# Optimization experiments

Hardware: AMD Instinct MI355X
Metric: run time of the kernel (lower is better)

Reference implementation:

```python
import jax, jax.numpy as jnp
import numpy as np
import math

EMB_DIM = 1024
HEAD_SIZE = 64
T = 4096
B = 4

def setup_inputs() -> dict:
    key = jax.random.key(0)
    k1, k2, k3, k4 = jax.random.split(key, 4)
    scale = 1.0 / math.sqrt(EMB_DIM)
    return {
        "input": jax.random.normal(k1, (B, T, EMB_DIM), dtype=jnp.float32),
        "Wq": jax.random.normal(k2, (EMB_DIM, HEAD_SIZE), dtype=jnp.float32) * scale,
        "Wk": jax.random.normal(k3, (EMB_DIM, HEAD_SIZE), dtype=jnp.float32) * scale,
        "Wv": jax.random.normal(k4, (EMB_DIM, HEAD_SIZE), dtype=jnp.float32) * scale,
    }

def reference(input, Wq, Wk, Wv):
    # q,k,v: [B,T,H]
    q = input @ Wq
    k = input @ Wk
    v = input @ Wv
    # scores: [B,T,T]
    match = jnp.einsum('bqh,bkh->bqk', q, k)
    # 'encoder' mask in this repo = causal tril mask
    causal = jnp.tril(jnp.ones((T, T), dtype=bool))
    match = jnp.where(causal, match, -jnp.inf)
    # NOTE: faithful to source quirk: softmax first, THEN divide by sqrt(head_size)
    attention = jax.nn.softmax(match, axis=-1) / math.sqrt(HEAD_SIZE)
    return jnp.einsum('bqk,bkh->bqh', attention, v)
```

## Files before the change

### kernel.cpp

```cpp
#include <hip/hip_runtime.h>

#define T_SEQ 4096
#define NBATCH 4
#define EMB 1024
#define HS 64
#define BT (NBATCH * T_SEQ)

typedef float f32x4 __attribute__((ext_vector_type(4)));
typedef short s16x8 __attribute__((ext_vector_type(8)));

__device__ __forceinline__ unsigned short f2bf(float x) {
  union { float f; unsigned u; } c; c.f = x;
  unsigned r = c.u + 0x7FFF + ((c.u >> 16) & 1);
  return (unsigned short)(r >> 16);
}
__device__ __forceinline__ float bf2f(unsigned short h) {
  union { unsigned u; float f; } c; c.u = ((unsigned)h) << 16;
  return c.f;
}
__device__ __forceinline__ void cvt8(float4 a0, float4 a1, s16x8& hi, s16x8& lo) {
  float xv[8] = {a0.x, a0.y, a0.z, a0.w, a1.x, a1.y, a1.z, a1.w};
#pragma unroll
  for (int j = 0; j < 8; ++j) {
    unsigned short h = f2bf(xv[j]);
    hi[j] = (short)h;
    lo[j] = (short)f2bf(xv[j] - bf2f(h));
  }
}

__global__ __launch_bounds__(256) void wconv(
    const float* __restrict__ Wq, const float* __restrict__ Wk,
    const float* __restrict__ Wv, unsigned short* __restrict__ wt_hi,
    unsigned short* __restrict__ wt_lo) {
  const int n3 = blockIdx.x;
  const int which = n3 >> 6, n = n3 & 63;
  const float* W = (which == 0) ? Wq : (which == 1) ? Wk : Wv;
#pragma unroll
  for (int i = 0; i < 4; ++i) {
    int k = i * 256 + threadIdx.x;
    float x = W[(size_t)k * HS + n];
    unsigned short h = f2bf(x);
    wt_hi[(size_t)n3 * EMB + k] = h;
    wt_lo[(size_t)n3 * EMB + k] = f2bf(x - bf2f(h));
  }
}

__global__ __launch_bounds__(512) void qkv_mfma(
    const float* __restrict__ inp, const unsigned short* __restrict__ wt_hi,
    const unsigned short* __restrict__ wt_lo, float* __restrict__ qf,
    unsigned short* __restrict__ khi, unsigned short* __restrict__ klo,
    unsigned short* __restrict__ vtb) {
  __shared__ unsigned short Bhi[192 * 40];
  __shared__ unsigned short Blo[192 * 40];
  const int t = threadIdx.x, lane = t & 63, w = t >> 6;
  const int m = lane & 15, quad = lane >> 4;
  const int mg = w >> 2, ng = w & 3;
  const int tok0 = blockIdx.x * 32;
  const int arow = tok0 + mg * 16 + m;

  f32x4 acc[3];
#pragma unroll
  for (int nt = 0; nt < 3; ++nt) acc[nt] = (f32x4){0.f, 0.f, 0.f, 0.f};

  const size_t offa = (size_t)(t >> 2) * EMB + (t & 3) * 8;
  const int idxb = (t < 256) ? (t + 512) : (t - 256);
  const unsigned short* srcb = (t < 256) ? wt_hi : wt_lo;
  const size_t offb = (size_t)(idxb >> 2) * EMB + (idxb & 3) * 8;
  const int idxc = t + 256;
  const size_t offc = (size_t)(idxc >> 2) * EMB + (idxc & 3) * 8;

  uint4 bpa, bpb, bpc;
  float4 apre0, apre1;
  bpa = *(const uint4*)&wt_hi[offa];
  bpb = *(const uint4*)&srcb[offb];
  bpc = *(const uint4*)&wt_lo[offc];
  {
    const float* ap = &inp[(size_t)arow * EMB + quad * 8];
    apre0 = *(const float4*)ap;
    apre1 = *(const float4*)(ap + 4);
  }

  for (int kc = 0; kc < 32; ++kc) {
    const int k0n = (kc + 1) * 32;
    __syncthreads();
    {
      *(uint4*)&Bhi[(t >> 2) * 40 + (t & 3) * 8] = bpa;
      unsigned short* dstb = (t < 256) ? Bhi : Blo;
      *(uint4*)&dstb[(idxb >> 2) * 40 + (idxb & 3) * 8] = bpb;
      *(uint4*)&Blo[(idxc >> 2) * 40 + (idxc & 3) * 8] = bpc;
    }
    __syncthreads();

    s16x8 ah, al;
    cvt8(apre0, apre1, ah, al);

    if (kc < 31) {
      bpa = *(const uint4*)&wt_hi[offa + k0n];
      bpb = *(const uint4*)&srcb[offb + k0n];
      bpc = *(const uint4*)&wt_lo[offc + k0n];
      const float* ap = &inp[(size_t)arow * EMB + k0n + quad * 8];
      apre0 = *(const float4*)ap;
      apre1 = *(const float4*)(ap + 4);
    }

#pragma unroll
    for (int nt = 0; nt < 3; ++nt) {
      int n3 = ng * 48 + nt * 16 + m;
      s16x8 bh = *(const s16x8*)&Bhi[n3 * 40 + quad * 8];
      s16x8 bl = *(const s16x8*)&Blo[n3 * 40 + quad * 8];
      acc[nt] = __builtin_amdgcn_mfma_f32_16x16x32_bf16(ah, bh, acc[nt], 0, 0, 0);
      acc[nt] = __builtin_amdgcn_mfma_f32_16x16x32_bf16(ah, bl, acc[nt], 0, 0, 0);
      acc[nt] = __builtin_amdgcn_mfma_f32_16x16x32_bf16(al, bh, acc[nt], 0, 0, 0);
    }
  }

#pragma unroll
  for (int nt = 0; nt < 3; ++nt) {
    int n3 = ng * 48 + nt * 16 + m;
    int which = n3 >> 6, col = n3 & 63;
#pragma unroll
    for (int r = 0; r < 4; ++r) {
      int tok = tok0 + mg * 16 + quad * 4 + r;
      float val = acc[nt][r];
      if (which == 0) {
        qf[(size_t)tok * HS + col] = val;
      } else if (which == 1) {
        unsigned short h = f2bf(val);
        khi[(size_t)tok * HS + col] = h;
        klo[(size_t)tok * HS + col] = f2bf(val - bf2f(h));
      } else {
        vtb[(size_t)(tok >> 6) * 4096 + (size_t)col * 64 + (tok & 63)] = f2bf(val);
      }
    }
  }
}

__global__ __launch_bounds__(256) void attn_part(
    const float* __restrict__ q, const unsigned short* __restrict__ khi,
    const unsigned short* __restrict__ klo, const unsigned short* __restrict__ vt,
    unsigned short* __restrict__ partO, float* __restrict__ partML) {
  __shared__ unsigned short Khi_s[64 * 72];
  __shared__ unsigned short Klo_s[64 * 72];
  __shared__ unsigned short Vt_s[64 * 72];
  __shared__ unsigned short P_s[4 * 16 * 72];
  const int t = threadIdx.x;
  const int lane = t & 63, w = t >> 6;
  const int m = lane & 15, quad = lane >> 4;

  int u = blockIdx.x;
  const int b = u / 160;
  u -= b * 160;
  int qtile = 0, c = 0;
  {
    int acc2 = 0;
    for (int qq = 0; qq < 64; ++qq) {
      int ncq = (qq >> 4) + 1;
      if (u < acc2 + ncq) { qtile = qq; c = u - acc2; break; }
      acc2 += ncq;
    }
  }
  const int kt0 = c * 16;
  const int kt1 = (kt0 + 16 < qtile + 1) ? kt0 + 16 : qtile + 1;

  const size_t qrow0 = (size_t)b * T_SEQ + (size_t)qtile * 64;
  const size_t krowbase = (size_t)b * T_SEQ;
  const int q_loc = w * 16 + m;

  s16x8 qh[2], ql[2];
#pragma unroll
  for (int cc = 0; cc < 2; ++cc) {
    const float* qp = &q[(qrow0 + q_loc) * HS + cc * 32 + quad * 8];
    cvt8(*(const float4*)qp, *(const float4*)(qp + 4), qh[cc], ql[cc]);
  }

  float l_st = 0.f;
  f32x4 o[4];
#pragma unroll
  for (int hb = 0; hb < 4; ++hb) o[hb] = (f32x4){0.f, 0.f, 0.f, 0.f};

  const int r0 = t >> 3, ch0 = t & 7;
  const int r1 = (256 + t) >> 3, ch1 = t & 7;

  uint4 pk0h, pk0l, pv0, pk1h, pk1l, pv1;
  {
    size_t g0 = (krowbase + (size_t)kt0 * 64 + r0) * HS + ch0 * 8;
    size_t g1 = (krowbase + (size_t)kt0 * 64 + r1) * HS + ch1 * 8;
    pk0h = *(const uint4*)&khi[g0]; pk0l = *(const uint4*)&klo[g0];
    pk1h = *(const uint4*)&khi[g1]; pk1l = *(const uint4*)&klo[g1];
    size_t v0 = (size_t)(b * 64 + kt0) * 4096 + (size_t)r0 * 64 + ch0 * 8;
    size_t v1 = (size_t)(b * 64 + kt0) * 4096 + (size_t)r1 * 64 + ch1 * 8;
    pv0 = *(const uint4*)&vt[v0]; pv1 = *(const uint4*)&vt[v1];
  }

  for (int kt = kt0; kt < kt1; ++kt) {
    __syncthreads();
    *(uint4*)&Khi_s[r0 * 72 + ch0 * 8] = pk0h;
    *(uint4*)&Klo_s[r0 * 72 + ch0 * 8] = pk0l;
    *(uint4*)&Vt_s[r0 * 72 + ch0 * 8] = pv0;
    *(uint4*)&Khi_s[r1 * 72 + ch1 * 8] = pk1h;
    *(uint4*)&Klo_s[r1 * 72 + ch1 * 8] = pk1l;
    *(uint4*)&Vt_s[r1 * 72 + ch1 * 8] = pv1;
    __syncthreads();

    if (kt + 1 < kt1) {
      size_t g0 = (krowbase + (size_t)(kt + 1) * 64 + r0) * HS + ch0 * 8;
      size_t g1 = (krowbase + (size_t)(kt + 1) * 64 + r1) * HS + ch1 * 8;
      pk0h = *(const uint4*)&khi[g0]; pk0l = *(const uint4*)&klo[g0];
      pk1h = *(const uint4*)&khi[g1]; pk1l = *(const uint4*)&klo[g1];
      size_t v0 = (size_t)(b * 64 + kt + 1) * 4096 + (size_t)r0 * 64 + ch0 * 8;
      size_t v1 = (size_t)(b * 64 + kt + 1) * 4096 + (size_t)r1 * 64 + ch1 * 8;
      pv0 = *(const uint4*)&vt[v0]; pv1 = *(const uint4*)&vt[v1];
    }

    f32x4 st[4];
#pragma unroll
    for (int cb = 0; cb < 4; ++cb) {
      st[cb] = (f32x4){0.f, 0.f, 0.f, 0.f};
#pragma unroll
      for (int cc = 0; cc < 2; ++cc) {
        s16x8 bh = *(const s16x8*)&Khi_s[(cb * 16 + m) * 72 + cc * 32 + quad * 8];
        s16x8 bl = *(const s16x8*)&Klo_s[(cb * 16 + m) * 72 + cc * 32 + quad * 8];
        st[cb] = __builtin_amdgcn_mfma_f32_16x16x32_bf16(bh, qh[cc], st[cb], 0, 0, 0);
        st[cb] = __builtin_amdgcn_mfma_f32_16x16x32_bf16(bl, qh[cc], st[cb], 0, 0, 0);
        st[cb] = __builtin_amdgcn_mfma_f32_16x16x32_bf16(bh, ql[cc], st[cb], 0, 0, 0);
      }
    }
    if (kt == qtile) {
#pragma unroll
      for (int cb = 0; cb < 4; ++cb)
#pragma unroll
        for (int r = 0; r < 4; ++r)
          if (cb * 16 + quad * 4 + r > q_loc) st[cb][r] = -1e30f;
    }
#pragma unroll
    for (int cb = 0; cb < 4; ++cb)
#pragma unroll
      for (int r = 0; r < 4; ++r) {
        st[cb][r] = __expf(st[cb][r]);
        l_st += st[cb][r];
      }
#pragma unroll
    for (int cb = 0; cb < 4; ++cb) {
      uint2 pk;
      pk.x = (unsigned)f2bf(st[cb][0]) | ((unsigned)f2bf(st[cb][1]) << 16);
      pk.y = (unsigned)f2bf(st[cb][2]) | ((unsigned)f2bf(st[cb][3]) << 16);
      *(uint2*)&P_s[q_loc * 72 + cb * 16 + quad * 4] = pk;
    }
    s16x8 pf[2];
#pragma unroll
    for (int cc = 0; cc < 2; ++cc)
      pf[cc] = *(const s16x8*)&P_s[q_loc * 72 + cc * 32 + quad * 8];
#pragma unroll
    for (int hb = 0; hb < 4; ++hb) {
#pragma unroll
      for (int cc = 0; cc < 2; ++cc) {
        s16x8 vf = *(const s16x8*)&Vt_s[(hb * 16 + m) * 72 + cc * 32 + quad * 8];
        o[hb] = __builtin_amdgcn_mfma_f32_16x16x32_bf16(vf, pf[cc], o[hb], 0, 0, 0);
      }
    }
  }

  l_st += __shfl_xor(l_st, 16, 64);
  l_st += __shfl_xor(l_st, 32, 64);

  const int slot = ((b * 64 + qtile) << 2) + c;
  unsigned short* Op = partO + (size_t)slot * 4096;
#pragma unroll
  for (int hb = 0; hb < 4; ++hb) {
    uint2 pk;
    pk.x = (unsigned)f2bf(o[hb][0]) | ((unsigned)f2bf(o[hb][1]) << 16);
    pk.y = (unsigned)f2bf(o[hb][2]) | ((unsigned)f2bf(o[hb][3]) << 16);
    *(uint2*)&Op[q_loc * 64 + hb * 16 + quad * 4] = pk;
  }
  if (quad == 0) partML[(size_t)slot * 64 + q_loc] = l_st;
}

__global__ __launch_bounds__(256) void attn_combine(
    const unsigned short* __restrict__ partO, const float* __restrict__ partML,
    float* __restrict__ out) {
  const int qtile = blockIdx.x, b = blockIdx.y;
  const int t = threadIdx.x;
  const int row = t >> 2, hg = t & 3;
  const int nc = (qtile >> 4) + 1;
  const int slot0 = (b * 64 + qtile) << 2;

  float lsum = 0.f;
  for (int i = 0; i < nc; ++i) lsum += partML[(size_t)(slot0 + i) * 64 + row];
  const float inv = 1.f / (lsum * 8.0f);

  float acc[16];
#pragma unroll
  for (int e = 0; e < 16; ++e) acc[e] = 0.f;
  for (int i = 0; i < nc; ++i) {
    const unsigned short* Op =
        partO + (size_t)(slot0 + i) * 4096 + row * 64 + hg * 16;
    uint4 u0 = *(const uint4*)Op;
    uint4 u1 = *(const uint4*)(Op + 8);
    unsigned uv[8] = {u0.x, u0.y, u0.z, u0.w, u1.x, u1.y, u1.z, u1.w};
#pragma unroll
    for (int e = 0; e < 8; ++e) {
      acc[2 * e] += bf2f((unsigned short)(uv[e] & 0xFFFF));
      acc[2 * e + 1] += bf2f((unsigned short)(uv[e] >> 16));
    }
  }
  float* op = &out[((size_t)b * T_SEQ + (size_t)qtile * 64 + row) * HS + hg * 16];
#pragma unroll
  for (int v = 0; v < 4; ++v) {
    float4 r;
    r.x = acc[4 * v + 0] * inv; r.y = acc[4 * v + 1] * inv;
    r.z = acc[4 * v + 2] * inv; r.w = acc[4 * v + 3] * inv;
    ((float4*)op)[v] = r;
  }
}

extern "C" void kernel_launch(void* const* d_in, const int* in_sizes, int n_in,
                              void* d_out, int out_size, void* d_ws, size_t ws_size,
                              hipStream_t stream) {
  const float* inp = (const float*)d_in[0];
  const float* Wq  = (const float*)d_in[1];
  const float* Wk  = (const float*)d_in[2];
  const float* Wv  = (const float*)d_in[3];
  float* out = (float*)d_out;

  char* base = (char*)d_ws;
  float* qf = (float*)base;
  unsigned short* khi = (unsigned short*)(base + (size_t)BT * HS * 4);
  unsigned short* klo = khi + (size_t)BT * HS;
  unsigned short* vtb = klo + (size_t)BT * HS;
  unsigned short* wt_hi = vtb + (size_t)BT * HS;
  unsigned short* wt_lo = wt_hi + (size_t)192 * EMB;
  unsigned short* partO = wt_lo + (size_t)192 * EMB;
  float* partML = (float*)(partO + (size_t)1024 * 4096);

  wconv<<<dim3(192), dim3(256), 0, stream>>>(Wq, Wk, Wv, wt_hi, wt_lo);
  qkv_mfma<<<dim3(BT / 32), dim3(512), 0, stream>>>(inp, wt_hi, wt_lo, qf, khi, klo, vtb);
  attn_part<<<dim3(640), dim3(256), 0, stream>>>(qf, khi, klo, vtb, partO, partML);
  attn_combine<<<dim3(64, NBATCH), dim3(256), 0, stream>>>(partO, partML, out);
}
```

Before: 190.6 us.

## Enlarge QKV projection tile to 64 tokens with split-K across wave pairs

The QKV projection kernel now handles 64 tokens per 1024-thread block. Each wave covers 96 output columns and half of the K dimension, and the two K halves are reduced through shared memory before the store. This halves how often the bf16 weight tiles are reloaded per token and halves the K-loop trip count. In exchange it needs a larger shared-memory footprint (about 54 KB), which may limit occupancy, and adds an extra barrier and LDS reduction step.

```diff
diff --git a/kernel.cpp b/kernel.cpp
--- a/kernel.cpp
+++ b/kernel.cpp
@@ -45,91 +45,118 @@
   }
 }
 
-__global__ __launch_bounds__(512) void qkv_mfma(
+__global__ __launch_bounds__(1024) void qkv_mfma(
     const float* __restrict__ inp, const unsigned short* __restrict__ wt_hi,
     const unsigned short* __restrict__ wt_lo, float* __restrict__ qf,
     unsigned short* __restrict__ khi, unsigned short* __restrict__ klo,
     unsigned short* __restrict__ vtb) {
-  __shared__ unsigned short Bhi[192 * 40];
-  __shared__ unsigned short Blo[192 * 40];
+  __shared__ __align__(16) char smem[55296];
+  unsigned short* Bs = (unsigned short*)smem;
+  float* Red = (float*)smem;
+
   const int t = threadIdx.x, lane = t & 63, w = t >> 6;
   const int m = lane & 15, quad = lane >> 4;
-  const int mg = w >> 2, ng = w & 3;
-  const int tok0 = blockIdx.x * 32;
+  const int mg = w >> 2, ng2 = (w >> 1) & 1, ks = w & 1;
+  const int tok0 = blockIdx.x * 64;
   const int arow = tok0 + mg * 16 + m;
 
-  f32x4 acc[3];
-#pragma unroll
-  for (int nt = 0; nt < 3; ++nt) acc[nt] = (f32x4){0.f, 0.f, 0.f, 0.f};
-
-  const size_t offa = (size_t)(t >> 2) * EMB + (t & 3) * 8;
-  const int idxb = (t < 256) ? (t + 512) : (t - 256);
-  const unsigned short* srcb = (t < 256) ? wt_hi : wt_lo;
-  const size_t offb = (size_t)(idxb >> 2) * EMB + (idxb & 3) * 8;
-  const int idxc = t + 256;
-  const size_t offc = (size_t)(idxc >> 2) * EMB + (idxc & 3) * 8;
+  f32x4 acc[6];
+#pragma unroll
+  for (int nt = 0; nt < 6; ++nt) acc[nt] = (f32x4){0.f, 0.f, 0.f, 0.f};
+
+  const int buf0 = (t < 768) ? 0 : 1;
+  const int idx0 = (t < 768) ? t : t - 768;
+  const int buf1 = (t < 512) ? 1 : 2;
+  const int idx1 = (t < 512) ? (256 + t) : (t - 512);
+  const int buf2 = (t < 256) ? 2 : 3;
+  const int idx2 = (t < 256) ? (512 + t) : (t - 256);
+  const unsigned short* src0 = (buf0 & 1) ? wt_lo : wt_hi;
+  const unsigned short* src1 = (buf1 & 1) ? wt_lo : wt_hi;
+  const unsigned short* src2 = (buf2 & 1) ? wt_lo : wt_hi;
+  const size_t off0 = (size_t)(idx0 >> 2) * EMB + (buf0 >> 1) * 512 + (idx0 & 3) * 8;
+  const size_t off1 = (size_t)(idx1 >> 2) * EMB + (buf1 >> 1) * 512 + (idx1 & 3) * 8;
+  const size_t off2 = (size_t)(idx2 >> 2) * EMB + (buf2 >> 1) * 512 + (idx2 & 3) * 8;
+  unsigned short* lds0 = Bs + buf0 * 6912 + (idx0 >> 2) * 36 + (idx0 & 3) * 8;
+  unsigned short* lds1 = Bs + buf1 * 6912 + (idx1 >> 2) * 36 + (idx1 & 3) * 8;
+  unsigned short* lds2 = Bs + buf2 * 6912 + (idx2 >> 2) * 36 + (idx2 & 3) * 8;
+
+  const unsigned short* Bhi_w = Bs + ks * 13824;
+  const unsigned short* Blo_w = Bs + 6912 + ks * 13824;
 
   uint4 bpa, bpb, bpc;
   float4 apre0, apre1;
-  bpa = *(const uint4*)&wt_hi[offa];
-  bpb = *(const uint4*)&srcb[offb];
-  bpc = *(const uint4*)&wt_lo[offc];
+  bpa = *(const uint4*)&src0[off0];
+  bpb = *(const uint4*)&src1[off1];
+  bpc = *(const uint4*)&src2[off2];
   {
-    const float* ap = &inp[(size_t)arow * EMB + quad * 8];
+    const float* ap = &inp[(size_t)arow * EMB + ks * 512 + quad * 8];
     apre0 = *(const float4*)ap;
     apre1 = *(const float4*)(ap + 4);
   }
 
-  for (int kc = 0; kc < 32; ++kc) {
+  for (int kc = 0; kc < 16; ++kc) {
     const int k0n = (kc + 1) * 32;
     __syncthreads();
-    {
-      *(uint4*)&Bhi[(t >> 2) * 40 + (t & 3) * 8] = bpa;
-      unsigned short* dstb = (t < 256) ? Bhi : Blo;
-      *(uint4*)&dstb[(idxb >> 2) * 40 + (idxb & 3) * 8] = bpb;
-      *(uint4*)&Blo[(idxc >> 2) * 40 + (idxc & 3) * 8] = bpc;
-    }
+    *(uint4*)lds0 = bpa;
+    *(uint4*)lds1 = bpb;
+    *(uint4*)lds2 = bpc;
     __syncthreads();
 
     s16x8 ah, al;
     cvt8(apre0, apre1, ah, al);
 
-    if (kc < 31) {
-      bpa = *(const uint4*)&wt_hi[offa + k0n];
-      bpb = *(const uint4*)&srcb[offb + k0n];
-      bpc = *(const uint4*)&wt_lo[offc + k0n];
-      const float* ap = &inp[(size_t)arow * EMB + k0n + quad * 8];
+    if (kc < 15) {
+      bpa = *(const uint4*)&src0[off0 + k0n];
+      bpb = *(const uint4*)&src1[off1 + k0n];
+      bpc = *(const uint4*)&src2[off2 + k0n];
+      const float* ap = &inp[(size_t)arow * EMB + ks * 512 + k0n + quad * 8];
       apre0 = *(const float4*)ap;
       apre1 = *(const float4*)(ap + 4);
     }
 
 #pragma unroll
-    for (int nt = 0; nt < 3; ++nt) {
-      int n3 = ng * 48 + nt * 16 + m;
-      s16x8 bh = *(const s16x8*)&Bhi[n3 * 40 + quad * 8];
-      s16x8 bl = *(const s16x8*)&Blo[n3 * 40 + quad * 8];
+    for (int nt = 0; nt < 6; ++nt) {
+      int n3 = ng2 * 96 + nt * 16 + m;
+      s16x8 bh = *(const s16x8*)&Bhi_w[n3 * 36 + quad * 8];
+      s16x8 bl = *(const s16x8*)&Blo_w[n3 * 36 + quad * 8];
       acc[nt] = __builtin_amdgcn_mfma_f32_16x16x32_bf16(ah, bh, acc[nt], 0, 0, 0);
       acc[nt] = __builtin_amdgcn_mfma_f32_16x16x32_bf16(ah, bl, acc[nt], 0, 0, 0);
       acc[nt] = __builtin_amdgcn_mfma_f32_16x16x32_bf16(al, bh, acc[nt], 0, 0, 0);
     }
   }
 
-#pragma unroll
-  for (int nt = 0; nt < 3; ++nt) {
-    int n3 = ng * 48 + nt * 16 + m;
-    int which = n3 >> 6, col = n3 & 63;
-#pragma unroll
-    for (int r = 0; r < 4; ++r) {
-      int tok = tok0 + mg * 16 + quad * 4 + r;
-      float val = acc[nt][r];
-      if (which == 0) {
-        qf[(size_t)tok * HS + col] = val;
-      } else if (which == 1) {
-        unsigned short h = f2bf(val);
-        khi[(size_t)tok * HS + col] = h;
-        klo[(size_t)tok * HS + col] = f2bf(val - bf2f(h));
-      } else {
-        vtb[(size_t)(tok >> 6) * 4096 + (size_t)col * 64 + (tok & 63)] = f2bf(val);
+  __syncthreads();
+  if (ks == 1) {
+#pragma unroll
+    for (int nt = 0; nt < 6; ++nt) {
+      int col = ng2 * 96 + nt * 16 + m;
+#pragma unroll
+      for (int r = 0; r < 4; ++r) {
+        int tok = mg * 16 + quad * 4 + r;
+        Red[tok * 196 + col] = acc[nt][r];
+      }
+    }
+  }
+  __syncthreads();
+  if (ks == 0) {
+#pragma unroll
+    for (int nt = 0; nt < 6; ++nt) {
+      int col = ng2 * 96 + nt * 16 + m;
+      int which = col >> 6, c3 = col & 63;
+#pragma unroll
+      for (int r = 0; r < 4; ++r) {
+        int tokl = mg * 16 + quad * 4 + r;
+        float val = acc[nt][r] + Red[tokl * 196 + col];
+        int tok = tok0 + tokl;
+        if (which == 0) {
+          qf[(size_t)tok * HS + c3] = val;
+        } else if (which == 1) {
+          unsigned short h = f2bf(val);
+          khi[(size_t)tok * HS + c3] = h;
+          klo[(size_t)tok * HS + c3] = f2bf(val - bf2f(h));
+        } else {
+          vtb[(size_t)(tok >> 6) * 4096 + (size_t)c3 * 64 + (tok & 63)] = f2bf(val);
+        }
       }
     }
   }
@@ -333,7 +360,7 @@
   float* partML = (float*)(partO + (size_t)1024 * 4096);
 
   wconv<<<dim3(192), dim3(256), 0, stream>>>(Wq, Wk, Wv, wt_hi, wt_lo);
-  qkv_mfma<<<dim3(BT / 32), dim3(512), 0, stream>>>(inp, wt_hi, wt_lo, qf, khi, klo, vtb);
+  qkv_mfma<<<dim3(BT / 64), dim3(1024), 0, stream>>>(inp, wt_hi, wt_lo, qf, khi, klo, vtb);
   attn_part<<<dim3(640), dim3(256), 0, stream>>>(qf, khi, klo, vtb, partO, partML);
   attn_combine<<<dim3(64, NBATCH), dim3(256), 0, stream>>>(partO, partML, out);
 }
```

New measurement: 242.1 us. 1.27x slower.
